# Performance work log

Hardware: AMD Instinct MI355X
Metric: run time of the kernel (lower is better)

Reference implementation:

```python
import jax, jax.numpy as jnp
import numpy as np

K = 3      # kernel_size
P = 1      # padding
NS = 2     # new_size = int(ratio*stride) = 2*1
GC = 16    # group_channels
G = 16     # groups = channels // group_channels
C = G * GC # 256
EPS = 1e-5


def _unfold(x):
    # torch.nn.Unfold(K, 1, P, 1): [B,C,H,W] -> [B,C,K,K,Ho,Wo], channel-major (C, kh, kw)
    B, Cc, H, W = x.shape
    xp = jnp.pad(x, ((0, 0), (0, 0), (P, P), (P, P)))
    rows = [jnp.stack([xp[:, :, i:i + H, j:j + W] for j in range(K)], axis=3)
            for i in range(K)]
    return jnp.stack(rows, axis=2)  # [B,C,K,K,H,W]


def _conv1x1(x, w, b=None):
    y = jnp.einsum('bihw,oi->bohw', x, w)
    if b is not None:
        y = y + b[None, :, None, None]
    return y


def reference(x, w1, bn_gamma, bn_beta, bn_mean, bn_var, w2, b2, w3, b3):
    B, Cc, H, W = x.shape
    xu = _unfold(x).reshape(B, G, GC, K, K, H, W)
    # three max-pooled descriptors
    x1 = jnp.max(xu.reshape(B, G, 4, GC // 4, K, K, H, W), axis=2).reshape(B, -1, H, W)
    x2 = jnp.max(xu, axis=3).reshape(B, -1, H, W)  # max over kh
    x3 = jnp.max(xu, axis=4).reshape(B, -1, H, W)  # max over kw
    w = jnp.concatenate([x1, x2, x3], axis=1)      # [B, G*(gc//4*K*K + 2*gc*K), H, W]
    # conv1 (1x1, no bias) + BN + ReLU
    w = _conv1x1(w, w1)
    inv = bn_gamma / jnp.sqrt(bn_var + EPS)
    w = w * inv[None, :, None, None] + (bn_beta - bn_mean * inv)[None, :, None, None]
    w = jax.nn.relu(w)
    # separable dynamic kernel: outer product over (kh,ns) x (kw,ns)
    wa = _conv1x1(w, w2, b2).reshape(B, G, 1, K, 1, NS, 1, H, W)
    wb = _conv1x1(w, w3, b3).reshape(B, G, 1, 1, K, 1, NS, H, W)
    wt = (wa * wb).reshape(B, G, 1, K * K, NS, NS, H, W)
    wt = jax.nn.softmax(wt, axis=3)
    # apply dynamic kernel: broadcast multiply, mean over K*K
    xv = xu.reshape(B, G, GC, K * K, 1, 1, H, W)
    out = jnp.mean(xv * wt, axis=3)                 # [B,G,GC,NS,NS,H,W]
    out = out.reshape(B, C, NS, NS, H, W)
    out = out.transpose(0, 1, 4, 2, 5, 3)           # [B,C,H,NS,W,NS]
    return out.reshape(B, C, H * NS, W * NS)


def setup_inputs() -> dict:
    key = jax.random.key(0)
    ks = jax.random.split(key, 6)
    in1 = G * (K * GC * 2 + K * K * (GC // 4))   # 2112
    out1 = G * NS * K                             # 96
    x = jax.random.normal(ks[0], (4, C, 56, 56), dtype=jnp.float32)
    w1 = jax.random.normal(ks[1], (out1, in1), dtype=jnp.float32) * 0.02
    w2 = jax.random.normal(ks[2], (out1, out1), dtype=jnp.float32) * 0.1
    b2 = jax.random.normal(ks[3], (out1,), dtype=jnp.float32) * 0.02
    w3 = jax.random.normal(ks[4], (out1, out1), dtype=jnp.float32) * 0.1
    b3 = jax.random.normal(ks[5], (out1,), dtype=jnp.float32) * 0.02
    return {
        'x': x, 'w1': w1,
        'bn_gamma': jnp.ones((out1,), jnp.float32),
        'bn_beta': jnp.zeros((out1,), jnp.float32),
        'bn_mean': jnp.zeros((out1,), jnp.float32),
        'bn_var': jnp.ones((out1,), jnp.float32),
        'w2': w2, 'b2': b2, 'w3': w3, 'b3': b3,
    }
```

## Files before the change

kernel.cpp:

```cpp
#include <hip/hip_runtime.h>

typedef __attribute__((ext_vector_type(8))) _Float16 half8;
typedef __attribute__((ext_vector_type(4))) _Float16 half4;
typedef __attribute__((ext_vector_type(4))) float floatx4;

__device__ inline void gld16(const _Float16* g, _Float16* lds) {
  __builtin_amdgcn_global_load_lds(
      (const __attribute__((address_space(1))) unsigned int*)g,
      (__attribute__((address_space(3))) unsigned int*)lds, 16, 0, 0);
}

__global__ __launch_bounds__(256) void kW(const float* __restrict__ w1,
                                          const float* __restrict__ w2,
                                          const float* __restrict__ w3,
                                          _Float16* __restrict__ w1f,
                                          _Float16* __restrict__ w2f,
                                          _Float16* __restrict__ w3f) {
  int i = blockIdx.x * 256 + threadIdx.x;
  if (i < 202752) w1f[i] = (_Float16)w1[i];
  else if (i < 211968) w2f[i - 202752] = (_Float16)w2[i - 202752];
  else if (i < 221184) w3f[i - 211968] = (_Float16)w3[i - 211968];
}

__global__ __launch_bounds__(512) void kDesc(const float* __restrict__ x,
                                             _Float16* __restrict__ descF) {
  int bid = blockIdx.x;
  int g = bid & 15;
  int h = (bid >> 4) % 56;
  int b = bid / 896;

  __shared__ __align__(16) _Float16 xb[144 * 72];
  __shared__ __align__(16) int tOf[132][4];
  __shared__ int tDg[132];

  const int t = threadIdx.x;

  if (t < 132) {
    int dl = t;
    int r0, r1, r2, r3, dg;
    if (dl < 36) {
      int a3 = dl / 9, rem = dl % 9, k1 = rem / 3, k2 = rem % 3;
      int br = (k2 * 3 + k1) * 16 + a3;
      r0 = br; r1 = br + 4; r2 = br + 8; r3 = br + 12;
      dg = g * 36 + dl;
    } else if (dl < 84) {
      int u = dl - 36, gc = u / 3, k2 = u % 3;
      r0 = (k2 * 3 + 0) * 16 + gc;
      r1 = (k2 * 3 + 1) * 16 + gc;
      r2 = (k2 * 3 + 2) * 16 + gc;
      r3 = r0;
      dg = 576 + g * 48 + u;
    } else {
      int u = dl - 84, gc = u / 3, k1 = u % 3;
      r0 = (0 + k1) * 16 + gc;
      r1 = (3 + k1) * 16 + gc;
      r2 = (6 + k1) * 16 + gc;
      r3 = r0;
      dg = 1344 + g * 48 + u;
    }
    tOf[dl][0] = r0 * 144 + ((r0 >> 4) & 7);
    tOf[dl][1] = r1 * 144 + ((r1 >> 4) & 7);
    tOf[dl][2] = r2 * 144 + ((r2 >> 4) & 7);
    tOf[dl][3] = r3 * 144 + ((r3 >> 4) & 7);
    tDg[dl] = dg;
  }

  {
    const long xp = ((long)b * 256 + g * 16) * 3136;
#pragma unroll
    for (int i = 0; i < 4; ++i) {
      int idx = t + i * 512;
      if (idx < 2016) {
        int r = idx / 14, c4 = idx - r * 14;
        int kk = r >> 4, ch = r & 15;
        int k2 = kk / 3, k1 = kk - 3 * k2;
        int t2 = k2 * 56 + h;
        int q3 = t2 / 3;
        int gr = q3 + k1 - 1;
        int s = t2 - q3 * 3;
        int col0 = c4 * 4;
        half4 hv;
        if (gr >= 0 && gr < 56) {
          long rb = xp + (long)ch * 3136 + (long)gr * 56 + (s - 1) + col0;
          bool interior = (col0 > 0 || s > 0) && (c4 < 13 || s < 2);
          if (interior) {
            float fv[4];
            __builtin_memcpy(fv, x + rb, 16);
            hv[0] = (_Float16)fv[0]; hv[1] = (_Float16)fv[1];
            hv[2] = (_Float16)fv[2]; hv[3] = (_Float16)fv[3];
          } else {
#pragma unroll
            for (int e = 0; e < 4; ++e) {
              int cg = col0 + e + s - 1;
              float v = 0.f;
              if ((unsigned)cg < 56u) v = x[rb + e];
              hv[e] = (_Float16)v;
            }
          }
        } else {
#pragma unroll
          for (int e = 0; e < 4; ++e) hv[e] = (_Float16)0.f;
        }
        int key = kk & 7;
        int chunk = (c4 >> 1) ^ key;
        *(half4*)((char*)xb + r * 144 + chunk * 16 + (c4 & 1) * 8) = hv;
      }
    }
  }
  __syncthreads();

  const long m00 = ((long)(b * 56 + h)) * 56;
#pragma unroll
  for (int i = 0; i < 2; ++i) {
    int idx = t + i * 512;
    if (idx < 924) {
      int pc = idx / 132, dl = idx - pc * 132;
      const int4 of = *(const int4*)tOf[dl];
      const char* xbb = (const char*)xb;
      half8 v0 = *(const half8*)(xbb + (of.x & ~15) + ((pc ^ (of.x & 15)) << 4));
      half8 v1 = *(const half8*)(xbb + (of.y & ~15) + ((pc ^ (of.y & 15)) << 4));
      half8 v2 = *(const half8*)(xbb + (of.z & ~15) + ((pc ^ (of.z & 15)) << 4));
      half8 v3 = *(const half8*)(xbb + (of.w & ~15) + ((pc ^ (of.w & 15)) << 4));
      half8 r8;
#pragma unroll
      for (int e = 0; e < 8; ++e) {
        _Float16 a = v0[e] > v1[e] ? v0[e] : v1[e];
        _Float16 c = v2[e] > v3[e] ? v2[e] : v3[e];
        r8[e] = a > c ? a : c;
      }
      _Float16* dp = descF + (m00 + pc * 8) * 2112 + tDg[dl];
#pragma unroll
      for (int e = 0; e < 8; ++e) dp[(long)e * 2112] = r8[e];
    }
  }
}

__global__ __launch_bounds__(256) void kGemm1(
    const _Float16* __restrict__ descF, const _Float16* __restrict__ w1f,
    _Float16* __restrict__ pacc) {
  __shared__ _Float16 Ab[2][64 * 32];
  __shared__ _Float16 Bb[2][96 * 32];
  const int t = threadIdx.x;
  const int wv = t >> 6, lane = t & 63, quad = lane >> 4, lr = lane & 15;
  const int mt = blockIdx.x / 11, ck = blockIdx.x % 11;
  const long mblk = (long)mt * 64;

  const long agbase = (mblk + (t >> 2)) * 2112 + ck * 192 + (t & 3) * 8;
  const long bg0 = (long)(t >> 2) * 2112 + ck * 192 + (t & 3) * 8;
  const long bg1 = (long)((256 + t) >> 2) * 2112 + ck * 192 + (t & 3) * 8;
  const int wslot = (t >> 6) * 512;

  floatx4 acc[6];
#pragma unroll
  for (int j = 0; j < 6; ++j) acc[j] = {0.f, 0.f, 0.f, 0.f};

  gld16(descF + agbase, &Ab[0][wslot]);
  gld16(w1f + bg0, &Bb[0][wslot]);
  if (t < 128) gld16(w1f + bg1, &Bb[0][2048 + wslot]);

  int buf = 0;
  for (int kt = 0; kt < 6; ++kt) {
    __syncthreads();
    if (kt < 5) {
      int off = (kt + 1) * 32;
      gld16(descF + agbase + off, &Ab[buf ^ 1][wslot]);
      gld16(w1f + bg0 + off, &Bb[buf ^ 1][wslot]);
      if (t < 128) gld16(w1f + bg1 + off, &Bb[buf ^ 1][2048 + wslot]);
    }
    half8 af = *(const half8*)(&Ab[buf][(wv * 16 + lr) * 32 + quad * 8]);
#pragma unroll
    for (int j = 0; j < 6; ++j) {
      half8 bf = *(const half8*)(&Bb[buf][(j * 16 + lr) * 32 + quad * 8]);
      acc[j] = __builtin_amdgcn_mfma_f32_16x16x32_f16(af, bf, acc[j], 0, 0, 0);
    }
    buf ^= 1;
  }

  _Float16* pp = pacc + (long)(ck * 196 + mt) * 6144;
#pragma unroll
  for (int j = 0; j < 6; ++j)
#pragma unroll
    for (int r = 0; r < 4; ++r)
      pp[(wv * 16 + quad * 4 + r) * 96 + j * 16 + lr] = (_Float16)acc[j][r];
}

__global__ __launch_bounds__(256) void kGemm2(
    const _Float16* __restrict__ pacc,
    const float* __restrict__ gamma, const float* __restrict__ beta,
    const float* __restrict__ mean, const float* __restrict__ var,
    const _Float16* __restrict__ w2f, const _Float16* __restrict__ w3f,
    const float* __restrict__ b2, const float* __restrict__ b3,
    _Float16* __restrict__ wtg) {
  __shared__ __align__(16) char smem[24576];
  _Float16* ytF = (_Float16*)smem;
  float* wal = (float*)smem;
  float* wbl = wal + 3072;
  __shared__ float invv[96], biasv[96];

  const int t = threadIdx.x;
  const int wv = t >> 6, lane = t & 63, quad = lane >> 4, lr = lane & 15;
  const int wr = wv & 1, wc = wv >> 1;
  const long mblk = (long)blockIdx.x * 32;

  if (t < 96) {
    float iv = gamma[t] * rsqrtf(var[t] + 1e-5f);
    invv[t] = iv; biasv[t] = beta[t] - mean[t] * iv;
  }
  __syncthreads();

#pragma unroll
  for (int i = 0; i < 3; ++i) {
    int q = t + i * 256;
    int m = q / 24, nq = (q - m * 24) * 4;
    long gbase = (mblk + m) * 96 + nq;
    float s0 = 0.f, s1 = 0.f, s2 = 0.f, s3 = 0.f;
#pragma unroll
    for (int ck = 0; ck < 11; ++ck) {
      half4 v = *(const half4*)(pacc + (long)ck * 1204224 + gbase);
      s0 += (float)v.x; s1 += (float)v.y; s2 += (float)v.z; s3 += (float)v.w;
    }
    half4 o;
    o.x = (_Float16)fmaxf(s0 * invv[nq + 0] + biasv[nq + 0], 0.f);
    o.y = (_Float16)fmaxf(s1 * invv[nq + 1] + biasv[nq + 1], 0.f);
    o.z = (_Float16)fmaxf(s2 * invv[nq + 2] + biasv[nq + 2], 0.f);
    o.w = (_Float16)fmaxf(s3 * invv[nq + 3] + biasv[nq + 3], 0.f);
    *(half4*)(ytF + m * 104 + nq) = o;
  }
  __syncthreads();

  floatx4 aa[3], ab[3];
#pragma unroll
  for (int j = 0; j < 3; ++j) { aa[j] = {0.f,0.f,0.f,0.f}; ab[j] = {0.f,0.f,0.f,0.f}; }
#pragma unroll
  for (int ks = 0; ks < 3; ++ks) {
    half8 af = *(const half8*)(ytF + (wr * 16 + lr) * 104 + ks * 32 + quad * 8);
#pragma unroll
    for (int j = 0; j < 3; ++j) {
      int n = (wc * 3 + j) * 16 + lr;
      int wo = n * 96 + ks * 32 + quad * 8;
      half8 b2v = *(const half8*)(w2f + wo);
      half8 b3v = *(const half8*)(w3f + wo);
      aa[j] = __builtin_amdgcn_mfma_f32_16x16x32_f16(af, b2v, aa[j], 0, 0, 0);
      ab[j] = __builtin_amdgcn_mfma_f32_16x16x32_f16(af, b3v, ab[j], 0, 0, 0);
    }
  }
  __syncthreads();

#pragma unroll
  for (int j = 0; j < 3; ++j) {
    int n = (wc * 3 + j) * 16 + lr;
    float bb2 = b2[n], bb3 = b3[n];
#pragma unroll
    for (int r = 0; r < 4; ++r) {
      int m = wr * 16 + quad * 4 + r;
      wal[m * 96 + n] = aa[j][r] + bb2;
      wbl[m * 96 + n] = ab[j][r] + bb3;
    }
  }
  __syncthreads();

#pragma unroll
  for (int it = 0; it < 8; ++it) {
    int u = t + it * 256;
    int m = u >> 6, rest = u & 63;
    int g = rest >> 2, ns = rest & 3;
    int ns1 = ns >> 1, ns2 = ns & 1;
    float la[3], lb[3];
#pragma unroll
    for (int k = 0; k < 3; ++k) {
      la[k] = wal[m * 96 + (g * 3 + k) * 2 + ns1];
      lb[k] = wbl[m * 96 + (g * 3 + k) * 2 + ns2];
    }
    float lg[9], mx = -1e30f;
#pragma unroll
    for (int k1 = 0; k1 < 3; ++k1)
#pragma unroll
      for (int k2 = 0; k2 < 3; ++k2) {
        float v = la[k1] * lb[k2];
        lg[k1 * 3 + k2] = v;
        mx = v > mx ? v : mx;
      }
    float s = 0.f;
#pragma unroll
    for (int k = 0; k < 9; ++k) { lg[k] = __expf(lg[k] - mx); s += lg[k]; }
    float sc = 1.f / (9.f * s);
    _Float16* dst = wtg + (mblk + m) * 576 + g * 36 + ns * 9;
#pragma unroll
    for (int k = 0; k < 9; ++k) dst[k] = (_Float16)(lg[k] * sc);
  }
}

__global__ __launch_bounds__(256) void kApply(const float* __restrict__ x,
                                              const _Float16* __restrict__ wt,
                                              float* __restrict__ out) {
  int bid = blockIdx.x;
  int g = bid & 15;
  int wh = (bid >> 4) & 1;
  int h = (bid >> 5) % 56;
  int b = bid / 1792;
  int wbase = wh * 28, cbase = g * 16;

  __shared__ _Float16 xr[9 * 16 * 30];
  __shared__ __align__(16) float wtb[28 * 36];
  __shared__ float ob[32 * 57];

  int t = threadIdx.x;

  {
    int wc = t & 31;
    int r0 = t >> 5;
    int wr = wbase + wc - 1;
    bool wok = (wc < 30) & (wr >= 0) & (wr < 56);
    const long xb0 = ((long)b * 256 + cbase) * 3136;
    float vals[18];
#pragma unroll
    for (int i = 0; i < 18; ++i) {
      int row = r0 + i * 8;
      int kk = row >> 4, cl = row & 15;
      int k2 = kk / 3, k1 = kk - 3 * k2;
      int gr = (k2 * 56 + h) / 3 + k1 - 1;
      float v = 0.f;
      if (wok && gr >= 0 && gr < 56)
        v = x[xb0 + (long)cl * 3136 + gr * 56 + wr];
      vals[i] = v;
    }
#pragma unroll
    for (int i = 0; i < 18; ++i) {
      int row = r0 + i * 8;
      if (wc < 30) xr[row * 30 + wc] = (_Float16)vals[i];
    }
  }
  {
    long m0 = ((long)(b * 56 + h)) * 56 + wbase;
    float vals[4];
#pragma unroll
    for (int i = 0; i < 4; ++i) {
      int idx = t + i * 256;
      if (idx < 1008) {
        int p = idx / 36, r36 = idx - p * 36;
        int kk = r36 >> 2, ns = r36 & 3;
        vals[i] = (float)wt[(m0 + p) * 576 + g * 36 + ns * 9 + kk];
      }
    }
#pragma unroll
    for (int i = 0; i < 4; ++i) {
      int idx = t + i * 256;
      if (idx < 1008) wtb[idx] = vals[i];
    }
  }
  __syncthreads();

  {
    int j2r[3];
#pragma unroll
    for (int k2 = 0; k2 < 3; ++k2) j2r[k2] = (k2 * 56 + h) % 3;
#pragma unroll
    for (int i = 0; i < 2; ++i) {
      int idx = i * 256 + t;
      int cl = idx & 15;
      int p = idx >> 4;
      if (p < 28) {
        float a0 = 0.f, a1 = 0.f, a2 = 0.f, a3 = 0.f;
#pragma unroll
        for (int k1 = 0; k1 < 3; ++k1)
#pragma unroll
          for (int k2 = 0; k2 < 3; ++k2) {
            float xv = (float)xr[(k2 * 3 + k1) * 480 + cl * 30 + p + j2r[k2]];
            float4 wv = *(const float4*)&wtb[p * 36 + (k1 * 3 + k2) * 4];
            a0 += xv * wv.x; a1 += xv * wv.y; a2 += xv * wv.z; a3 += xv * wv.w;
          }
        int ob0 = cl * 114 + p * 2;
        ob[ob0] = a0;
        ob[ob0 + 1] = a1;
        ob[ob0 + 57] = a2;
        ob[ob0 + 58] = a3;
      }
    }
  }
  __syncthreads();

  {
    int wo = t & 63;
    int r0 = t >> 6;
    const long obase = (((long)b * 256 + cbase) * 112 + 2 * h) * 112 + wh * 56;
#pragma unroll
    for (int i = 0; i < 8; ++i) {
      int row = r0 + i * 4;
      if (wo < 56) {
        int cli = row >> 1, n1 = row & 1;
        out[obase + cli * 12544 + n1 * 112 + wo] = ob[row * 57 + wo];
      }
    }
  }
}

extern "C" void kernel_launch(void* const* d_in, const int* in_sizes, int n_in,
                              void* d_out, int out_size, void* d_ws, size_t ws_size,
                              hipStream_t stream) {
  const float* x = (const float*)d_in[0];
  const float* w1 = (const float*)d_in[1];
  const float* gamma = (const float*)d_in[2];
  const float* beta = (const float*)d_in[3];
  const float* mean = (const float*)d_in[4];
  const float* var = (const float*)d_in[5];
  const float* w2 = (const float*)d_in[6];
  const float* b2 = (const float*)d_in[7];
  const float* w3 = (const float*)d_in[8];
  const float* b3 = (const float*)d_in[9];
  float* out = (float*)d_out;

  _Float16* w1f = (_Float16*)d_ws;
  _Float16* w2f = w1f + 202752;
  _Float16* w3f = w2f + 9216;
  _Float16* wtg = (_Float16*)((char*)d_ws + 442368);
  _Float16* descF = (_Float16*)((char*)d_ws + 14893056);
  _Float16* pacc = (_Float16*)((char*)d_ws + 67878912);

  hipLaunchKernelGGL(kW, dim3(864), dim3(256), 0, stream, w1, w2, w3, w1f, w2f, w3f);
  hipLaunchKernelGGL(kDesc, dim3(3584), dim3(512), 0, stream, x, descF);
  hipLaunchKernelGGL(kGemm1, dim3(2156), dim3(256), 0, stream, descF, w1f, pacc);
  hipLaunchKernelGGL(kGemm2, dim3(392), dim3(256), 0, stream,
                     pacc, gamma, beta, mean, var, w2f, w3f, b2, b3, wtg);
  hipLaunchKernelGGL(kApply, dim3(7168), dim3(256), 0, stream, x, wtg, out);
}
```

Before: 187.8 us.

## Fuse weight conversion into descriptor kernel and double-buffer groups per block

```diff
diff --git a/kernel.cpp b/kernel.cpp
--- a/kernel.cpp
+++ b/kernel.cpp
@@ -10,128 +10,156 @@
       (__attribute__((address_space(3))) unsigned int*)lds, 16, 0, 0);
 }
 
-__global__ __launch_bounds__(256) void kW(const float* __restrict__ w1,
-                                          const float* __restrict__ w2,
-                                          const float* __restrict__ w3,
-                                          _Float16* __restrict__ w1f,
-                                          _Float16* __restrict__ w2f,
-                                          _Float16* __restrict__ w3f) {
-  int i = blockIdx.x * 256 + threadIdx.x;
-  if (i < 202752) w1f[i] = (_Float16)w1[i];
-  else if (i < 211968) w2f[i - 202752] = (_Float16)w2[i - 202752];
-  else if (i < 221184) w3f[i - 211968] = (_Float16)w3[i - 211968];
-}
-
-__global__ __launch_bounds__(512) void kDesc(const float* __restrict__ x,
-                                             _Float16* __restrict__ descF) {
-  int bid = blockIdx.x;
-  int g = bid & 15;
-  int h = (bid >> 4) % 56;
-  int b = bid / 896;
-
-  __shared__ __align__(16) _Float16 xb[144 * 72];
+__device__ __forceinline__ void descCalc(const float* __restrict__ x, long xp, int h,
+                                         int idx, half4& hv, int& off) {
+  int r = idx / 14, c4 = idx - r * 14;
+  int kk = r >> 4, ch = r & 15;
+  int k2 = kk / 3, k1 = kk - 3 * k2;
+  int t2 = k2 * 56 + h;
+  int q3 = t2 / 3;
+  int gr = q3 + k1 - 1;
+  int s = t2 - q3 * 3;
+  int col0 = c4 * 4;
+  hv[0] = hv[1] = hv[2] = hv[3] = (_Float16)0.f;
+  if (gr >= 0 && gr < 56) {
+    long rb = xp + (long)ch * 3136 + (long)gr * 56 + (s - 1) + col0;
+    bool interior = (col0 > 0 || s > 0) && (c4 < 13 || s < 2);
+    if (interior) {
+      float fv[4];
+      __builtin_memcpy(fv, x + rb, 16);
+      hv[0] = (_Float16)fv[0]; hv[1] = (_Float16)fv[1];
+      hv[2] = (_Float16)fv[2]; hv[3] = (_Float16)fv[3];
+    } else {
+#pragma unroll
+      for (int e = 0; e < 4; ++e) {
+        int cg = col0 + e + s - 1;
+        float v = 0.f;
+        if ((unsigned)cg < 56u) v = x[rb + e];
+        hv[e] = (_Float16)v;
+      }
+    }
+  }
+  off = r * 144 + (((c4 >> 1) ^ (kk & 7)) << 4) + (c4 & 1) * 8;
+}
+
+__global__ __launch_bounds__(512) void kDescW(const float* __restrict__ x,
+                                              const float* __restrict__ w1,
+                                              const float* __restrict__ w2,
+                                              const float* __restrict__ w3,
+                                              _Float16* __restrict__ descF,
+                                              _Float16* __restrict__ w1f,
+                                              _Float16* __restrict__ w2f,
+                                              _Float16* __restrict__ w3f) {
+  __shared__ __align__(16) _Float16 xb[2][144 * 72];
   __shared__ __align__(16) int tOf[132][4];
-  __shared__ int tDg[132];
 
   const int t = threadIdx.x;
+  const int bid = blockIdx.x;
+
+  if (bid >= 896) {
+    int i = (bid - 896) * 512 + t;
+    if (i < 202752) w1f[i] = (_Float16)w1[i];
+    else if (i < 211968) w2f[i - 202752] = (_Float16)w2[i - 202752];
+    else if (i < 221184) w3f[i - 211968] = (_Float16)w3[i - 211968];
+    return;
+  }
+
+  const int gq = bid & 3;
+  const int rest = bid >> 2;
+  const int h = rest % 56;
+  const int b = rest / 56;
 
   if (t < 132) {
     int dl = t;
-    int r0, r1, r2, r3, dg;
+    int r0, r1, r2, r3;
     if (dl < 36) {
       int a3 = dl / 9, rem = dl % 9, k1 = rem / 3, k2 = rem % 3;
       int br = (k2 * 3 + k1) * 16 + a3;
       r0 = br; r1 = br + 4; r2 = br + 8; r3 = br + 12;
-      dg = g * 36 + dl;
     } else if (dl < 84) {
       int u = dl - 36, gc = u / 3, k2 = u % 3;
       r0 = (k2 * 3 + 0) * 16 + gc;
       r1 = (k2 * 3 + 1) * 16 + gc;
       r2 = (k2 * 3 + 2) * 16 + gc;
       r3 = r0;
-      dg = 576 + g * 48 + u;
     } else {
       int u = dl - 84, gc = u / 3, k1 = u % 3;
       r0 = (0 + k1) * 16 + gc;
       r1 = (3 + k1) * 16 + gc;
       r2 = (6 + k1) * 16 + gc;
       r3 = r0;
-      dg = 1344 + g * 48 + u;
     }
     tOf[dl][0] = r0 * 144 + ((r0 >> 4) & 7);
     tOf[dl][1] = r1 * 144 + ((r1 >> 4) & 7);
     tOf[dl][2] = r2 * 144 + ((r2 >> 4) & 7);
     tOf[dl][3] = r3 * 144 + ((r3 >> 4) & 7);
-    tDg[dl] = dg;
   }
 
   {
-    const long xp = ((long)b * 256 + g * 16) * 3136;
+    const int g0 = gq * 4;
+    const long xp = ((long)b * 256 + g0 * 16) * 3136;
 #pragma unroll
     for (int i = 0; i < 4; ++i) {
       int idx = t + i * 512;
       if (idx < 2016) {
-        int r = idx / 14, c4 = idx - r * 14;
-        int kk = r >> 4, ch = r & 15;
-        int k2 = kk / 3, k1 = kk - 3 * k2;
-        int t2 = k2 * 56 + h;
-        int q3 = t2 / 3;
-        int gr = q3 + k1 - 1;
-        int s = t2 - q3 * 3;
-        int col0 = c4 * 4;
-        half4 hv;
-        if (gr >= 0 && gr < 56) {
-          long rb = xp + (long)ch * 3136 + (long)gr * 56 + (s - 1) + col0;
-          bool interior = (col0 > 0 || s > 0) && (c4 < 13 || s < 2);
-          if (interior) {
-            float fv[4];
-            __builtin_memcpy(fv, x + rb, 16);
-            hv[0] = (_Float16)fv[0]; hv[1] = (_Float16)fv[1];
-            hv[2] = (_Float16)fv[2]; hv[3] = (_Float16)fv[3];
-          } else {
-#pragma unroll
-            for (int e = 0; e < 4; ++e) {
-              int cg = col0 + e + s - 1;
-              float v = 0.f;
-              if ((unsigned)cg < 56u) v = x[rb + e];
-              hv[e] = (_Float16)v;
-            }
-          }
-        } else {
-#pragma unroll
-          for (int e = 0; e < 4; ++e) hv[e] = (_Float16)0.f;
-        }
-        int key = kk & 7;
-        int chunk = (c4 >> 1) ^ key;
-        *(half4*)((char*)xb + r * 144 + chunk * 16 + (c4 & 1) * 8) = hv;
+        half4 hv; int off;
+        descCalc(x, xp, h, idx, hv, off);
+        *(half4*)((char*)xb[0] + off) = hv;
       }
     }
   }
   __syncthreads();
 
   const long m00 = ((long)(b * 56 + h)) * 56;
-#pragma unroll
-  for (int i = 0; i < 2; ++i) {
-    int idx = t + i * 512;
-    if (idx < 924) {
-      int pc = idx / 132, dl = idx - pc * 132;
-      const int4 of = *(const int4*)tOf[dl];
-      const char* xbb = (const char*)xb;
-      half8 v0 = *(const half8*)(xbb + (of.x & ~15) + ((pc ^ (of.x & 15)) << 4));
-      half8 v1 = *(const half8*)(xbb + (of.y & ~15) + ((pc ^ (of.y & 15)) << 4));
-      half8 v2 = *(const half8*)(xbb + (of.z & ~15) + ((pc ^ (of.z & 15)) << 4));
-      half8 v3 = *(const half8*)(xbb + (of.w & ~15) + ((pc ^ (of.w & 15)) << 4));
-      half8 r8;
-#pragma unroll
-      for (int e = 0; e < 8; ++e) {
-        _Float16 a = v0[e] > v1[e] ? v0[e] : v1[e];
-        _Float16 c = v2[e] > v3[e] ? v2[e] : v3[e];
-        r8[e] = a > c ? a : c;
-      }
-      _Float16* dp = descF + (m00 + pc * 8) * 2112 + tDg[dl];
-#pragma unroll
-      for (int e = 0; e < 8; ++e) dp[(long)e * 2112] = r8[e];
-    }
+  int cur = 0;
+#pragma unroll
+  for (int gi = 0; gi < 4; ++gi) {
+    const int g = gq * 4 + gi;
+
+    half4 pv0, pv1, pv2, pv3;
+    int po0 = -1, po1 = -1, po2 = -1, po3 = -1;
+    if (gi < 3) {
+      const long xp = ((long)b * 256 + (g + 1) * 16) * 3136;
+      {
+        int idx = t;            descCalc(x, xp, h, idx, pv0, po0);
+      }
+      { int idx = t + 512;      descCalc(x, xp, h, idx, pv1, po1); }
+      { int idx = t + 1024;     descCalc(x, xp, h, idx, pv2, po2); }
+      { int idx = t + 1536;     if (idx < 2016) descCalc(x, xp, h, idx, pv3, po3); else po3 = -1; }
+    }
+
+#pragma unroll
+    for (int i = 0; i < 2; ++i) {
+      int idx = t + i * 512;
+      if (idx < 924) {
+        int pc = idx / 132, dl = idx - pc * 132;
+        const int4 of = *(const int4*)tOf[dl];
+        const char* xbb = (const char*)xb[cur];
+        half8 v0 = *(const half8*)(xbb + (of.x & ~15) + ((pc ^ (of.x & 15)) << 4));
+        half8 v1 = *(const half8*)(xbb + (of.y & ~15) + ((pc ^ (of.y & 15)) << 4));
+        half8 v2 = *(const half8*)(xbb + (of.z & ~15) + ((pc ^ (of.z & 15)) << 4));
+        half8 v3 = *(const half8*)(xbb + (of.w & ~15) + ((pc ^ (of.w & 15)) << 4));
+        half8 a = __builtin_elementwise_max(v0, v1);
+        half8 c = __builtin_elementwise_max(v2, v3);
+        half8 r8 = __builtin_elementwise_max(a, c);
+        int dg = (dl < 36) ? (g * 36 + dl)
+               : (dl < 84) ? (576 + g * 48 + (dl - 36))
+                           : (1344 + g * 48 + (dl - 84));
+        _Float16* dp = descF + (m00 + pc * 8) * 2112 + dg;
+#pragma unroll
+        for (int e = 0; e < 8; ++e) dp[(long)e * 2112] = r8[e];
+      }
+    }
+
+    if (gi < 3) {
+      char* dst = (char*)xb[cur ^ 1];
+      *(half4*)(dst + po0) = pv0;
+      *(half4*)(dst + po1) = pv1;
+      *(half4*)(dst + po2) = pv2;
+      if (po3 >= 0) *(half4*)(dst + po3) = pv3;
+    }
+    __syncthreads();
+    cur ^= 1;
   }
 }
 
@@ -416,8 +444,8 @@
   _Float16* descF = (_Float16*)((char*)d_ws + 14893056);
   _Float16* pacc = (_Float16*)((char*)d_ws + 67878912);
 
-  hipLaunchKernelGGL(kW, dim3(864), dim3(256), 0, stream, w1, w2, w3, w1f, w2f, w3f);
-  hipLaunchKernelGGL(kDesc, dim3(3584), dim3(512), 0, stream, x, descF);
+  hipLaunchKernelGGL(kDescW, dim3(1328), dim3(512), 0, stream,
+                     x, w1, w2, w3, descF, w1f, w2f, w3f);
   hipLaunchKernelGGL(kGemm1, dim3(2156), dim3(256), 0, stream, descF, w1f, pacc);
   hipLaunchKernelGGL(kGemm2, dim3(392), dim3(256), 0, stream,
                      pacc, gamma, beta, mean, var, w2f, w3f, b2, b3, wtg);
```

After: 185.1 us. Within noise of the previous version (-1.4%).

## Merge weight-cast kernel into descriptor kernel and vectorize descriptor stores

Applied to the files above, without the earlier changes.

```diff
diff --git a/kernel.cpp b/kernel.cpp
--- a/kernel.cpp
+++ b/kernel.cpp
@@ -2,6 +2,7 @@
 
 typedef __attribute__((ext_vector_type(8))) _Float16 half8;
 typedef __attribute__((ext_vector_type(4))) _Float16 half4;
+typedef __attribute__((ext_vector_type(2))) _Float16 half2v;
 typedef __attribute__((ext_vector_type(4))) float floatx4;
 
 __device__ inline void gld16(const _Float16* g, _Float16* lds) {
@@ -10,66 +11,63 @@
       (__attribute__((address_space(3))) unsigned int*)lds, 16, 0, 0);
 }
 
-__global__ __launch_bounds__(256) void kW(const float* __restrict__ w1,
-                                          const float* __restrict__ w2,
-                                          const float* __restrict__ w3,
-                                          _Float16* __restrict__ w1f,
-                                          _Float16* __restrict__ w2f,
-                                          _Float16* __restrict__ w3f) {
-  int i = blockIdx.x * 256 + threadIdx.x;
-  if (i < 202752) w1f[i] = (_Float16)w1[i];
-  else if (i < 211968) w2f[i - 202752] = (_Float16)w2[i - 202752];
-  else if (i < 221184) w3f[i - 211968] = (_Float16)w3[i - 211968];
-}
-
-__global__ __launch_bounds__(512) void kDesc(const float* __restrict__ x,
-                                             _Float16* __restrict__ descF) {
-  int bid = blockIdx.x;
+__global__ __launch_bounds__(256) void kDescC(const float* __restrict__ x,
+                                              const float* __restrict__ w1,
+                                              const float* __restrict__ w2,
+                                              const float* __restrict__ w3,
+                                              _Float16* __restrict__ descF,
+                                              _Float16* __restrict__ w1f,
+                                              _Float16* __restrict__ w2f,
+                                              _Float16* __restrict__ w3f) {
+  const int bid = blockIdx.x;
+  const int t = threadIdx.x;
+
+  if (bid >= 3584) {
+    int i = (bid - 3584) * 256 + t;
+    if (i < 202752) w1f[i] = (_Float16)w1[i];
+    else if (i < 211968) w2f[i - 202752] = (_Float16)w2[i - 202752];
+    else if (i < 221184) w3f[i - 211968] = (_Float16)w3[i - 211968];
+    return;
+  }
+
   int g = bid & 15;
   int h = (bid >> 4) % 56;
   int b = bid / 896;
 
   __shared__ __align__(16) _Float16 xb[144 * 72];
   __shared__ __align__(16) int tOf[132][4];
-  __shared__ int tDg[132];
-
-  const int t = threadIdx.x;
 
   if (t < 132) {
     int dl = t;
-    int r0, r1, r2, r3, dg;
+    int r0, r1, r2, r3;
     if (dl < 36) {
       int a3 = dl / 9, rem = dl % 9, k1 = rem / 3, k2 = rem % 3;
       int br = (k2 * 3 + k1) * 16 + a3;
       r0 = br; r1 = br + 4; r2 = br + 8; r3 = br + 12;
-      dg = g * 36 + dl;
     } else if (dl < 84) {
       int u = dl - 36, gc = u / 3, k2 = u % 3;
       r0 = (k2 * 3 + 0) * 16 + gc;
       r1 = (k2 * 3 + 1) * 16 + gc;
       r2 = (k2 * 3 + 2) * 16 + gc;
       r3 = r0;
-      dg = 576 + g * 48 + u;
     } else {
       int u = dl - 84, gc = u / 3, k1 = u % 3;
       r0 = (0 + k1) * 16 + gc;
       r1 = (3 + k1) * 16 + gc;
       r2 = (6 + k1) * 16 + gc;
       r3 = r0;
-      dg = 1344 + g * 48 + u;
     }
     tOf[dl][0] = r0 * 144 + ((r0 >> 4) & 7);
     tOf[dl][1] = r1 * 144 + ((r1 >> 4) & 7);
     tOf[dl][2] = r2 * 144 + ((r2 >> 4) & 7);
     tOf[dl][3] = r3 * 144 + ((r3 >> 4) & 7);
-    tDg[dl] = dg;
   }
 
   {
     const long xp = ((long)b * 256 + g * 16) * 3136;
 #pragma unroll
-    for (int i = 0; i < 4; ++i) {
-      int idx = t + i * 512;
+    for (int i = 0; i < 8; ++i) {
+      int idx = t + i * 256;
       if (idx < 2016) {
         int r = idx / 14, c4 = idx - r * 14;
         int kk = r >> 4, ch = r & 15;
@@ -110,27 +108,31 @@
   __syncthreads();
 
   const long m00 = ((long)(b * 56 + h)) * 56;
-#pragma unroll
-  for (int i = 0; i < 2; ++i) {
-    int idx = t + i * 512;
-    if (idx < 924) {
-      int pc = idx / 132, dl = idx - pc * 132;
-      const int4 of = *(const int4*)tOf[dl];
-      const char* xbb = (const char*)xb;
+  if (t < 231) {
+    int pc = t / 33, dlc = t - pc * 33;
+    int dl0 = dlc * 4;
+    half8 r8s[4];
+    const char* xbb = (const char*)xb;
+#pragma unroll
+    for (int i = 0; i < 4; ++i) {
+      const int4 of = *(const int4*)tOf[dl0 + i];
       half8 v0 = *(const half8*)(xbb + (of.x & ~15) + ((pc ^ (of.x & 15)) << 4));
       half8 v1 = *(const half8*)(xbb + (of.y & ~15) + ((pc ^ (of.y & 15)) << 4));
       half8 v2 = *(const half8*)(xbb + (of.z & ~15) + ((pc ^ (of.z & 15)) << 4));
       half8 v3 = *(const half8*)(xbb + (of.w & ~15) + ((pc ^ (of.w & 15)) << 4));
-      half8 r8;
-#pragma unroll
-      for (int e = 0; e < 8; ++e) {
-        _Float16 a = v0[e] > v1[e] ? v0[e] : v1[e];
-        _Float16 c = v2[e] > v3[e] ? v2[e] : v3[e];
-        r8[e] = a > c ? a : c;
-      }
-      _Float16* dp = descF + (m00 + pc * 8) * 2112 + tDg[dl];
-#pragma unroll
-      for (int e = 0; e < 8; ++e) dp[(long)e * 2112] = r8[e];
+      half8 a = __builtin_elementwise_max(v0, v1);
+      half8 c = __builtin_elementwise_max(v2, v3);
+      r8s[i] = __builtin_elementwise_max(a, c);
+    }
+    int dg0 = (dlc < 9)  ? (g * 36 + dl0)
+            : (dlc < 21) ? (576 + g * 48 + (dl0 - 36))
+                         : (1344 + g * 48 + (dl0 - 84));
+    _Float16* dp = descF + (m00 + pc * 8) * 2112 + dg0;
+#pragma unroll
+    for (int e = 0; e < 8; ++e) {
+      half4 o;
+      o[0] = r8s[0][e]; o[1] = r8s[1][e]; o[2] = r8s[2][e]; o[3] = r8s[3][e];
+      *(half4*)(dp + (long)e * 2112) = o;
     }
   }
 }
@@ -416,8 +418,8 @@
   _Float16* descF = (_Float16*)((char*)d_ws + 14893056);
   _Float16* pacc = (_Float16*)((char*)d_ws + 67878912);
 
-  hipLaunchKernelGGL(kW, dim3(864), dim3(256), 0, stream, w1, w2, w3, w1f, w2f, w3f);
-  hipLaunchKernelGGL(kDesc, dim3(3584), dim3(512), 0, stream, x, descF);
+  hipLaunchKernelGGL(kDescC, dim3(4448), dim3(256), 0, stream,
+                     x, w1, w2, w3, descF, w1f, w2f, w3f);
   hipLaunchKernelGGL(kGemm1, dim3(2156), dim3(256), 0, stream, descF, w1f, pacc);
   hipLaunchKernelGGL(kGemm2, dim3(392), dim3(256), 0, stream,
                      pacc, gamma, beta, mean, var, w2f, w3f, b2, b3, wtg);
```

After: 182.6 us. 2.7% less time.
